# Kernel optimization log

Hardware: AMD Instinct MI355X
Metric: run time of the kernel (lower is better)

The kernel has to match this reference:

```python
import jax, jax.numpy as jnp
import numpy as np

BITS = 4
GROUPSIZE = 128
IN_F = 4096
OUT_F = 11008
VALS_PER_I32 = 32 // BITS  # 8
MASK = (1 << BITS) - 1     # 0xF


def _dequant_weight(qweight, qzeros, scales):
    """GPTQ 4-bit dequant. qweight: [K//8, N] int32 packed along K;
    qzeros: [G, N//8] int32 packed along N; scales: [G, N].
    Returns float32 weight [K, N]."""
    shifts = (jnp.arange(VALS_PER_I32, dtype=jnp.uint32) * BITS)
    # unpack weights: each int32 row holds 8 consecutive K-rows
    qw = qweight.astype(jnp.uint32)                              # [K//8, N]
    w_int = ((qw[:, None, :] >> shifts[None, :, None]) & MASK)   # [K//8, 8, N]
    w_int = w_int.reshape(IN_F, OUT_F)                           # [K, N]
    # unpack zeros: each int32 col holds 8 consecutive N-cols; stored zeros = z - 1
    qz = qzeros.astype(jnp.uint32)                               # [G, N//8]
    z_int = ((qz[:, :, None] >> shifts[None, None, :]) & MASK)   # [G, N//8, 8]
    n_groups = qzeros.shape[0]
    z_int = z_int.reshape(n_groups, OUT_F) + 1                   # [G, N]
    # per-group dequant: w = scales[g] * (q - z[g])
    g_idx = jnp.arange(IN_F) // GROUPSIZE                        # [K]
    w = (w_int.astype(jnp.float32) - z_int.astype(jnp.float32)[g_idx]) * scales[g_idx]
    return w                                                     # [K, N]


def setup_inputs() -> dict:
    key = jax.random.key(0)
    k1, k2, k3, k4, k5 = jax.random.split(key, 5)
    n_groups = IN_F // GROUPSIZE
    x = jax.random.normal(k1, (4, IN_F), dtype=jnp.float32)
    scales = jax.random.uniform(k2, (n_groups, OUT_F), dtype=jnp.float32,
                                minval=0.001, maxval=0.01)
    bias = jax.random.normal(k3, (OUT_F,), dtype=jnp.float32)
    qweight = jax.random.randint(k4, (IN_F // 32 * BITS, OUT_F), 0, 2147483647,
                                 dtype=jnp.int32)
    qzeros = jax.random.randint(k5, (n_groups, OUT_F // 256 * (BITS * 8)), 0,
                                2147483647, dtype=jnp.int32)
    return {"x": x, "scales": scales, "bias": bias,
            "qweight": qweight, "qzeros": qzeros}


def reference(x, scales, bias, qweight, qzeros):
    w = _dequant_weight(qweight, qzeros, scales)    # [K, N] float32
    y = x.astype(jnp.float32) @ w + bias            # [tokens, N]
    return y.astype(x.dtype)
```

## Files before the change

### kernel.cpp

```cpp
#include <hip/hip_runtime.h>

typedef float v2f __attribute__((ext_vector_type(2)));

#define IN_F 4096
#define OUT_F 11008
#define GROUPSIZE 128
#define NGROUPS 32
#define QROWS 512
#define ZCOLS 1376

#define TILE_N 128
#define NTILES 86
#define WS_NEW_BYTES ((size_t)NGROUPS * 4 * OUT_F * sizeof(float))
#define WS_OLD_BYTES ((size_t)8 * 4 * OUT_F * sizeof(float))

__global__ __launch_bounds__(256) void gptq_s1(
    const float* __restrict__ x,
    const float* __restrict__ scales,
    const int*   __restrict__ qweight,
    const int*   __restrict__ qzeros,
    float*       __restrict__ ws)
{
    __shared__ float red[4][4][TILE_N];

    const int tid  = threadIdx.x;
    const int lane = tid & 63;
    const int kq   = __builtin_amdgcn_readfirstlane(tid >> 6);
    const int bx   = blockIdx.x;
    const int g    = blockIdx.y;
    const int c0   = bx * TILE_N + lane * 2;

    const unsigned qz = (unsigned)qzeros[g * ZCOLS + (c0 >> 3)];
    const unsigned sh = 4u * (unsigned)(c0 & 7);
    const float z0 = (float)(((qz >> sh) & 0xFu) + 1u);
    const float z1 = (float)(((qz >> (sh + 4u)) & 0xFu) + 1u);
    const v2f sc = *(const v2f*)(scales + g * OUT_F + c0);

    const int r0 = g * 16 + kq * 4;

    const int2 w0 = *(const int2*)(qweight + (r0 + 0) * OUT_F + c0);
    const int2 w1 = *(const int2*)(qweight + (r0 + 1) * OUT_F + c0);
    const int2 w2 = *(const int2*)(qweight + (r0 + 2) * OUT_F + c0);
    const int2 w3 = *(const int2*)(qweight + (r0 + 3) * OUT_F + c0);
    const int2 ww[4] = {w0, w1, w2, w3};

    float acc0[4] = {0.f, 0.f, 0.f, 0.f};
    float acc1[4] = {0.f, 0.f, 0.f, 0.f};

    #pragma unroll
    for (int t = 0; t < 4; ++t) {
        const unsigned wa = (unsigned)ww[t].x;
        const unsigned wb = (unsigned)ww[t].y;
        const unsigned la = wa & 0x0F0F0F0Fu, ha = (wa >> 4) & 0x0F0F0F0Fu;
        const unsigned lb = wb & 0x0F0F0F0Fu, hb = (wb >> 4) & 0x0F0F0F0Fu;
        float qa[8], qb[8];
        qa[0] = (float)(la & 0xFFu);         qa[1] = (float)(ha & 0xFFu);
        qa[2] = (float)((la >> 8) & 0xFFu);  qa[3] = (float)((ha >> 8) & 0xFFu);
        qa[4] = (float)((la >> 16) & 0xFFu); qa[5] = (float)((ha >> 16) & 0xFFu);
        qa[6] = (float)(la >> 24);           qa[7] = (float)(ha >> 24);
        qb[0] = (float)(lb & 0xFFu);         qb[1] = (float)(hb & 0xFFu);
        qb[2] = (float)((lb >> 8) & 0xFFu);  qb[3] = (float)((hb >> 8) & 0xFFu);
        qb[4] = (float)((lb >> 16) & 0xFFu); qb[5] = (float)((hb >> 16) & 0xFFu);
        qb[6] = (float)(lb >> 24);           qb[7] = (float)(hb >> 24);

        const int k0 = (r0 + t) * 8;
        #pragma unroll
        for (int j = 0; j < 8; ++j) {
            const float d0 = qa[j] - z0;
            const float d1 = qb[j] - z1;
            #pragma unroll
            for (int m = 0; m < 4; ++m) {
                const float xf = x[m * IN_F + k0 + j];
                acc0[m] += xf * d0;
                acc1[m] += xf * d1;
            }
        }
    }

    #pragma unroll
    for (int m = 0; m < 4; ++m) {
        v2f r;
        r.x = acc0[m] * sc.x;
        r.y = acc1[m] * sc.y;
        *(v2f*)&red[kq][m][lane * 2] = r;
    }
    __syncthreads();

    const int o = tid * 2;
    const int m = o >> 7;
    const int c = o & 127;
    const float* rb = &red[0][m][c];
    v2f p = *(const v2f*)rb;
    #pragma unroll
    for (int k = 1; k < 4; ++k) {
        const v2f q = *(const v2f*)(rb + k * 4 * TILE_N);
        p.x += q.x;
        p.y += q.y;
    }
    *(v2f*)(ws + (size_t)(g * 4 + m) * OUT_F + bx * TILE_N + c) = p;
}

__global__ __launch_bounds__(256) void gptq_s2(
    const float* __restrict__ ws,
    const float* __restrict__ bias,
    float*       __restrict__ out)
{
    const int n = blockIdx.x * 256 + threadIdx.x;
    const int m = blockIdx.y;
    float s0 = bias[n], s1 = 0.f, s2 = 0.f, s3 = 0.f;
    #pragma unroll
    for (int g = 0; g < NGROUPS; g += 4) {
        s0 += ws[(size_t)((g + 0) * 4 + m) * OUT_F + n];
        s1 += ws[(size_t)((g + 1) * 4 + m) * OUT_F + n];
        s2 += ws[(size_t)((g + 2) * 4 + m) * OUT_F + n];
        s3 += ws[(size_t)((g + 3) * 4 + m) * OUT_F + n];
    }
    out[m * OUT_F + n] = (s0 + s1) + (s2 + s3);
}

__global__ __launch_bounds__(256) void gptq_partial_kernel(
    const float* __restrict__ x, const float* __restrict__ scales,
    const int* __restrict__ qweight, const int* __restrict__ qzeros,
    float* __restrict__ ws)
{
    __shared__ float part[4][4][64];
    const int tid = threadIdx.x;
    const int col = tid & 63;
    const int kp  = tid >> 6;
    const int n   = blockIdx.x * 64 + col;
    const int g   = blockIdx.y * 4 + kp;
    const int gu  = __builtin_amdgcn_readfirstlane(g);
    const unsigned qz = (unsigned)qzeros[g * ZCOLS + (n >> 3)];
    const float zf = (float)(((qz >> (4u * (unsigned)(n & 7))) & 0xFu) + 1u);
    const float sc = scales[g * OUT_F + n];
    float ga[4] = {0.f, 0.f, 0.f, 0.f};
    const int kkbase = gu * (GROUPSIZE / 8);
    #pragma unroll
    for (int t = 0; t < GROUPSIZE / 8; ++t) {
        const int kk = kkbase + t;
        const unsigned w = (unsigned)qweight[kk * OUT_F + n];
        const unsigned lo = w & 0x0F0F0F0Fu;
        const unsigned hi = (w >> 4) & 0x0F0F0F0Fu;
        float q[8];
        q[0] = (float)(lo & 0xFFu);         q[1] = (float)(hi & 0xFFu);
        q[2] = (float)((lo >> 8) & 0xFFu);  q[3] = (float)((hi >> 8) & 0xFFu);
        q[4] = (float)((lo >> 16) & 0xFFu); q[5] = (float)((hi >> 16) & 0xFFu);
        q[6] = (float)(lo >> 24);           q[7] = (float)(hi >> 24);
        const int k0 = kk * 8;
        #pragma unroll
        for (int j = 0; j < 8; ++j) {
            const float d = q[j] - zf;
            #pragma unroll
            for (int m = 0; m < 4; ++m) ga[m] += x[m * IN_F + k0 + j] * d;
        }
    }
    #pragma unroll
    for (int m = 0; m < 4; ++m) part[kp][m][col] = sc * ga[m];
    __syncthreads();
    const int m = tid >> 6;
    const int c = tid & 63;
    const int nn = blockIdx.x * 64 + c;
    const float s = part[0][m][c] + part[1][m][c] + part[2][m][c] + part[3][m][c];
    ws[(blockIdx.y * 4 + m) * OUT_F + nn] = s;
}

__global__ __launch_bounds__(256) void gptq_reduce_kernel(
    const float* __restrict__ ws, const float* __restrict__ bias,
    float* __restrict__ out)
{
    const int n = blockIdx.x * 256 + threadIdx.x;
    const int m = blockIdx.y;
    float s = bias[n];
    #pragma unroll
    for (int ks = 0; ks < 8; ++ks) s += ws[(ks * 4 + m) * OUT_F + n];
    out[m * OUT_F + n] = s;
}

extern "C" void kernel_launch(void* const* d_in, const int* in_sizes, int n_in,
                              void* d_out, int out_size, void* d_ws, size_t ws_size,
                              hipStream_t stream) {
    const float* x       = (const float*)d_in[0];
    const float* scales  = (const float*)d_in[1];
    const float* bias    = (const float*)d_in[2];
    const int*   qweight = (const int*)d_in[3];
    const int*   qzeros  = (const int*)d_in[4];
    float*       out     = (float*)d_out;

    if (ws_size >= WS_NEW_BYTES) {
        float* ws = (float*)d_ws;
        dim3 g1(NTILES, NGROUPS);
        gptq_s1<<<g1, 256, 0, stream>>>(x, scales, qweight, qzeros, ws);
        dim3 g2(OUT_F / 256, 4);
        gptq_s2<<<g2, 256, 0, stream>>>(ws, bias, out);
    } else if (ws_size >= WS_OLD_BYTES) {
        float* ws = (float*)d_ws;
        dim3 g1(OUT_F / 64, 8);
        gptq_partial_kernel<<<g1, 256, 0, stream>>>(x, scales, qweight, qzeros, ws);
        dim3 g2(OUT_F / 256, 4);
        gptq_reduce_kernel<<<g2, 256, 0, stream>>>(ws, bias, out);
    }
}
```

Measured before the change: 17.53 us.

## Remap stage-1 threads to one packed row by four columns with register-held x

The first-stage kernel now gives each thread one packed qweight row and four consecutive output columns, loaded as a single int4, instead of four rows by two columns. The eight x values per token for that row are loaded once as float4 vectors into registers rather than re-read inside the inner loop. Tiles shrink to 64 columns, so the grid grows to 172 blocks per group and the shared-memory reduction now sums 16 row partials instead of 4. This trades larger vector loads and fewer x loads for a bigger LDS reduction and more blocks.

Result: slower. 19.63 us (+12.0%).

```diff
diff --git a/kernel.cpp b/kernel.cpp
--- a/kernel.cpp
+++ b/kernel.cpp
@@ -1,6 +1,4 @@
 #include <hip/hip_runtime.h>
-
-typedef float v2f __attribute__((ext_vector_type(2)));
 
 #define IN_F 4096
 #define OUT_F 11008
@@ -9,95 +7,93 @@
 #define QROWS 512
 #define ZCOLS 1376
 
-#define TILE_N 128
-#define NTILES 86
 #define WS_NEW_BYTES ((size_t)NGROUPS * 4 * OUT_F * sizeof(float))
 #define WS_OLD_BYTES ((size_t)8 * 4 * OUT_F * sizeof(float))
 
-__global__ __launch_bounds__(256) void gptq_s1(
+__global__ __launch_bounds__(256) void gptq_s1_reg(
     const float* __restrict__ x,
     const float* __restrict__ scales,
     const int*   __restrict__ qweight,
     const int*   __restrict__ qzeros,
     float*       __restrict__ ws)
 {
-    __shared__ float red[4][4][TILE_N];
+    __shared__ float part[16][4][64];
 
-    const int tid  = threadIdx.x;
-    const int lane = tid & 63;
-    const int kq   = __builtin_amdgcn_readfirstlane(tid >> 6);
-    const int bx   = blockIdx.x;
-    const int g    = blockIdx.y;
-    const int c0   = bx * TILE_N + lane * 2;
+    const int tid = threadIdx.x;
+    const int rl  = tid >> 4;
+    const int cq  = tid & 15;
+    const int bx  = blockIdx.x;
+    const int g   = blockIdx.y;
+    const int c0  = bx * 64 + cq * 4;
+    const int row = g * 16 + rl;
+    const int k0  = row * 8;
 
+    const int4 w4 = *(const int4*)(qweight + (size_t)row * OUT_F + c0);
     const unsigned qz = (unsigned)qzeros[g * ZCOLS + (c0 >> 3)];
-    const unsigned sh = 4u * (unsigned)(c0 & 7);
-    const float z0 = (float)(((qz >> sh) & 0xFu) + 1u);
-    const float z1 = (float)(((qz >> (sh + 4u)) & 0xFu) + 1u);
-    const v2f sc = *(const v2f*)(scales + g * OUT_F + c0);
+    const float4 s4 = *(const float4*)(scales + g * OUT_F + c0);
+    float4 xa[4], xb[4];
+    #pragma unroll
+    for (int m = 0; m < 4; ++m) {
+        xa[m] = *(const float4*)(x + m * IN_F + k0);
+        xb[m] = *(const float4*)(x + m * IN_F + k0 + 4);
+    }
 
-    const int r0 = g * 16 + kq * 4;
+    const unsigned bsh = 4u * (unsigned)(c0 & 7);
+    const unsigned wv[4] = {(unsigned)w4.x, (unsigned)w4.y,
+                            (unsigned)w4.z, (unsigned)w4.w};
 
-    const int2 w0 = *(const int2*)(qweight + (r0 + 0) * OUT_F + c0);
-    const int2 w1 = *(const int2*)(qweight + (r0 + 1) * OUT_F + c0);
-    const int2 w2 = *(const int2*)(qweight + (r0 + 2) * OUT_F + c0);
-    const int2 w3 = *(const int2*)(qweight + (r0 + 3) * OUT_F + c0);
-    const int2 ww[4] = {w0, w1, w2, w3};
-
-    float acc0[4] = {0.f, 0.f, 0.f, 0.f};
-    float acc1[4] = {0.f, 0.f, 0.f, 0.f};
+    float acc[4][4];
+    #pragma unroll
+    for (int m = 0; m < 4; ++m)
+        #pragma unroll
+        for (int c = 0; c < 4; ++c) acc[m][c] = 0.f;
 
     #pragma unroll
-    for (int t = 0; t < 4; ++t) {
-        const unsigned wa = (unsigned)ww[t].x;
-        const unsigned wb = (unsigned)ww[t].y;
-        const unsigned la = wa & 0x0F0F0F0Fu, ha = (wa >> 4) & 0x0F0F0F0Fu;
-        const unsigned lb = wb & 0x0F0F0F0Fu, hb = (wb >> 4) & 0x0F0F0F0Fu;
-        float qa[8], qb[8];
-        qa[0] = (float)(la & 0xFFu);         qa[1] = (float)(ha & 0xFFu);
-        qa[2] = (float)((la >> 8) & 0xFFu);  qa[3] = (float)((ha >> 8) & 0xFFu);
-        qa[4] = (float)((la >> 16) & 0xFFu); qa[5] = (float)((ha >> 16) & 0xFFu);
-        qa[6] = (float)(la >> 24);           qa[7] = (float)(ha >> 24);
-        qb[0] = (float)(lb & 0xFFu);         qb[1] = (float)(hb & 0xFFu);
-        qb[2] = (float)((lb >> 8) & 0xFFu);  qb[3] = (float)((hb >> 8) & 0xFFu);
-        qb[4] = (float)((lb >> 16) & 0xFFu); qb[5] = (float)((hb >> 16) & 0xFFu);
-        qb[6] = (float)(lb >> 24);           qb[7] = (float)(hb >> 24);
-
-        const int k0 = (r0 + t) * 8;
+    for (int c = 0; c < 4; ++c) {
+        const float z = (float)(((qz >> (bsh + 4u * c)) & 0xFu) + 1u);
+        const unsigned w  = wv[c];
+        const unsigned lo = w & 0x0F0F0F0Fu;
+        const unsigned hi = (w >> 4) & 0x0F0F0F0Fu;
+        float d[8];
+        d[0] = (float)(lo & 0xFFu) - z;          d[1] = (float)(hi & 0xFFu) - z;
+        d[2] = (float)((lo >> 8) & 0xFFu) - z;   d[3] = (float)((hi >> 8) & 0xFFu) - z;
+        d[4] = (float)((lo >> 16) & 0xFFu) - z;  d[5] = (float)((hi >> 16) & 0xFFu) - z;
+        d[6] = (float)(lo >> 24) - z;            d[7] = (float)(hi >> 24) - z;
         #pragma unroll
-        for (int j = 0; j < 8; ++j) {
-            const float d0 = qa[j] - z0;
-            const float d1 = qb[j] - z1;
-            #pragma unroll
-            for (int m = 0; m < 4; ++m) {
-                const float xf = x[m * IN_F + k0 + j];
-                acc0[m] += xf * d0;
-                acc1[m] += xf * d1;
-            }
+        for (int m = 0; m < 4; ++m) {
+            acc[m][c] += xa[m].x * d[0];
+            acc[m][c] += xa[m].y * d[1];
+            acc[m][c] += xa[m].z * d[2];
+            acc[m][c] += xa[m].w * d[3];
+            acc[m][c] += xb[m].x * d[4];
+            acc[m][c] += xb[m].y * d[5];
+            acc[m][c] += xb[m].z * d[6];
+            acc[m][c] += xb[m].w * d[7];
         }
     }
 
     #pragma unroll
     for (int m = 0; m < 4; ++m) {
-        v2f r;
-        r.x = acc0[m] * sc.x;
-        r.y = acc1[m] * sc.y;
-        *(v2f*)&red[kq][m][lane * 2] = r;
+        float4 r;
+        r.x = acc[m][0] * s4.x;
+        r.y = acc[m][1] * s4.y;
+        r.z = acc[m][2] * s4.z;
+        r.w = acc[m][3] * s4.w;
+        *(float4*)&part[rl][m][cq * 4] = r;
     }
     __syncthreads();
 
-    const int o = tid * 2;
-    const int m = o >> 7;
-    const int c = o & 127;
-    const float* rb = &red[0][m][c];
-    v2f p = *(const v2f*)rb;
+    const int m   = tid >> 6;
+    const int col = tid & 63;
+    float t0 = 0.f, t1 = 0.f, t2 = 0.f, t3 = 0.f;
     #pragma unroll
-    for (int k = 1; k < 4; ++k) {
-        const v2f q = *(const v2f*)(rb + k * 4 * TILE_N);
-        p.x += q.x;
-        p.y += q.y;
+    for (int r = 0; r < 16; r += 4) {
+        t0 += part[r + 0][m][col];
+        t1 += part[r + 1][m][col];
+        t2 += part[r + 2][m][col];
+        t3 += part[r + 3][m][col];
     }
-    *(v2f*)(ws + (size_t)(g * 4 + m) * OUT_F + bx * TILE_N + c) = p;
+    ws[(size_t)(g * 4 + m) * OUT_F + bx * 64 + col] = (t0 + t1) + (t2 + t3);
 }
 
 __global__ __launch_bounds__(256) void gptq_s2(
@@ -164,7 +160,7 @@
     ws[(blockIdx.y * 4 + m) * OUT_F + nn] = s;
 }
 
-__global__ __launch_bounds__(256) void gptq_reduce_kernel(
+__global__ __launch_bounds__(256) void gptq_reduce8(
     const float* __restrict__ ws, const float* __restrict__ bias,
     float* __restrict__ out)
 {
@@ -188,8 +184,8 @@
 
     if (ws_size >= WS_NEW_BYTES) {
         float* ws = (float*)d_ws;
-        dim3 g1(NTILES, NGROUPS);
-        gptq_s1<<<g1, 256, 0, stream>>>(x, scales, qweight, qzeros, ws);
+        dim3 g1(OUT_F / 64, NGROUPS);
+        gptq_s1_reg<<<g1, 256, 0, stream>>>(x, scales, qweight, qzeros, ws);
         dim3 g2(OUT_F / 256, 4);
         gptq_s2<<<g2, 256, 0, stream>>>(ws, bias, out);
     } else if (ws_size >= WS_OLD_BYTES) {
@@ -197,6 +193,6 @@
         dim3 g1(OUT_F / 64, 8);
         gptq_partial_kernel<<<g1, 256, 0, stream>>>(x, scales, qweight, qzeros, ws);
         dim3 g2(OUT_F / 256, 4);
-        gptq_reduce_kernel<<<g2, 256, 0, stream>>>(ws, bias, out);
+        gptq_reduce8<<<g2, 256, 0, stream>>>(ws, bias, out);
     }
 }
```
